# Kernel optimization log

Hardware: AMD Instinct MI355X
Metric: run time of the kernel (lower is better)

Reference implementation:

```python
import jax, jax.numpy as jnp
import numpy as np

NUM_TABLES = 26
NUM_ROWS = 50000
WIDTH = 128
BATCH = 4096
NNZ = 20
NUM_NUM = 13
MLP_SIZES = [512, 256, 128]


def setup_inputs() -> dict:
    key = jax.random.key(0)
    ks = jax.random.split(key, 16)
    numerical = jax.random.normal(ks[0], (BATCH, NUM_NUM), dtype=jnp.float32)
    cat = jax.random.randint(ks[1], (NUM_TABLES, BATCH, NNZ), 0, NUM_ROWS)
    tables = jax.random.normal(ks[2], (NUM_TABLES, NUM_ROWS, WIDTH), dtype=jnp.float32) * 0.01
    d_in = NUM_TABLES * WIDTH + NUM_NUM  # concat of pooled embeddings + numericals
    dims = [d_in] + MLP_SIZES + [1]
    inp = {"numerical": numerical, "cat": cat, "tables": tables}
    for i in range(len(dims) - 1):
        scale = 1.0 / np.sqrt(dims[i])
        inp[f"W{i+1}"] = jax.random.normal(ks[3 + i], (dims[i], dims[i + 1]), dtype=jnp.float32) * scale
        inp[f"b{i+1}"] = jnp.zeros((dims[i + 1],), dtype=jnp.float32)
    return inp


def reference(numerical, cat, tables, W1, b1, W2, b2, W3, b3, W4, b4):
    # Multi-table gather + reduce_sum: tables [T,R,W], cat [T,B,NNZ] -> pooled [T,B,W]
    pooled = jax.vmap(lambda T, idx: jnp.take(T, idx, axis=0).sum(axis=1))(tables, cat)
    # concat pooled tables (in input order) then numericals: [B, T*W + NUM_NUM]
    flat = pooled.transpose(1, 0, 2).reshape(pooled.shape[1], -1)
    x = jnp.concatenate([flat, numerical], axis=1)
    x = jax.nn.relu(x @ W1 + b1)
    x = jax.nn.relu(x @ W2 + b2)
    x = jax.nn.relu(x @ W3 + b3)
    return x @ W4 + b4  # [B, 1]
```

## Files before the change

### kernel.cpp

```cpp
#include <hip/hip_runtime.h>
#include <hip/hip_bf16.h>

#define T_NUM_TABLES 26
#define T_NUM_ROWS 50000
#define T_WIDTH 128
#define T_BATCH 4096
#define T_NNZ 20
#define T_NUM_NUM 13
#define T_DE (T_NUM_TABLES * T_WIDTH)

typedef __attribute__((ext_vector_type(4))) float f32x4;
typedef __attribute__((ext_vector_type(8))) short bf16x8;

__global__ void prep_v5(const float* __restrict__ W1, const float* __restrict__ W2,
                        const float* __restrict__ W3, const float* __restrict__ b1,
                        const float* __restrict__ b4, const float* __restrict__ num,
                        __hip_bfloat16* __restrict__ w1t, __hip_bfloat16* __restrict__ w2t,
                        __hip_bfloat16* __restrict__ w3t, float* __restrict__ c0,
                        float* __restrict__ out) {
  int bid = blockIdx.x;
  if (bid >= 1824) {
    int b = bid - 1824;
    __shared__ float snum[T_NUM_NUM];
    if (threadIdx.x < T_NUM_NUM) snum[threadIdx.x] = num[b * T_NUM_NUM + threadIdx.x];
    if (threadIdx.x == 0) out[b] = b4[0];
    __syncthreads();
#pragma unroll
    for (int rep = 0; rep < 2; ++rep) {
      int n = threadIdx.x + rep * 256;
      float acc = b1[n];
#pragma unroll
      for (int j = 0; j < T_NUM_NUM; ++j)
        acc += snum[j] * W1[(size_t)(T_DE + j) * 512 + n];
      c0[(size_t)b * 512 + n] = acc;
    }
    return;
  }
  const float* in;
  __hip_bfloat16* outt;
  int Kc, N, xb, yb;
  if (bid < 1664)      { in = W1; outt = w1t; Kc = 3328; N = 512; xb = bid % 104; yb = bid / 104; }
  else if (bid < 1792) { int r = bid - 1664; in = W2; outt = w2t; Kc = 512; N = 256; xb = r % 16; yb = r / 16; }
  else                 { int r = bid - 1792; in = W3; outt = w3t; Kc = 256; N = 128; xb = r % 8;  yb = r / 8;  }
  int tx = threadIdx.x & 31, ty = threadIdx.x >> 5;
  __shared__ float tile[32][33];
  int kb = xb * 32, nb = yb * 32;
  for (int r = ty; r < 32; r += 8) tile[r][tx] = in[(size_t)(kb + r) * N + nb + tx];
  __syncthreads();
  for (int r = ty; r < 32; r += 8) outt[(size_t)(nb + r) * Kc + kb + tx] = __float2bfloat16(tile[tx][r]);
}

__global__ void pool_v5(const float* __restrict__ tables,
                        const int* __restrict__ cat,
                        __hip_bfloat16* __restrict__ xh) {
  __shared__ int sidx[8][T_NNZ];
  const int b0 = blockIdx.x * 8;
  const int t = blockIdx.y;
  const int tx = threadIdx.x & 31;
  const int ty = threadIdx.x >> 5;
  if (threadIdx.x < 8 * T_NNZ) {
    int y = threadIdx.x / T_NNZ, j = threadIdx.x % T_NNZ;
    sidx[y][j] = cat[((size_t)t * T_BATCH + b0 + y) * T_NNZ + j];
  }
  __syncthreads();
  const f32x4* tb = (const f32x4*)(tables + (size_t)t * T_NUM_ROWS * T_WIDTH);
  f32x4 acc = {0.f, 0.f, 0.f, 0.f};
#pragma unroll
  for (int j = 0; j < T_NNZ; ++j) {
    acc += tb[(size_t)sidx[ty][j] * 32 + tx];
  }
  ushort4 u;
  {
    __hip_bfloat16 h0 = __float2bfloat16(acc[0]), h1 = __float2bfloat16(acc[1]);
    __hip_bfloat16 h2 = __float2bfloat16(acc[2]), h3 = __float2bfloat16(acc[3]);
    u.x = *(unsigned short*)&h0; u.y = *(unsigned short*)&h1;
    u.z = *(unsigned short*)&h2; u.w = *(unsigned short*)&h3;
  }
  *(ushort4*)(&xh[(size_t)(b0 + ty) * T_DE + t * T_WIDTH + tx * 4]) = u;
}

template <int BM, int BN, int RELU, int MODE>
__global__ __launch_bounds__(256, 2) void gemm_v5(
    const __hip_bfloat16* __restrict__ A,
    const __hip_bfloat16* __restrict__ Bt,
    const float* __restrict__ bias1,
    const float* __restrict__ bias2d,
    const float* __restrict__ W4,
    __hip_bfloat16* __restrict__ Ch,
    float* __restrict__ outv,
    int M, int N, int Kp) {
  constexpr int MR = BM / 32, NR = BN / 32;
  __shared__ char smem[BM * 128 + BN * 128];
  char* As = smem;
  char* Bs = smem + BM * 128;

  const int tid = threadIdx.x;
  const int wave = tid >> 6;
  const int lane = tid & 63;
  const int m0 = blockIdx.x * BM;
  const int n0 = blockIdx.y * BN;
  const int wr = wave >> 1;
  const int wc = wave & 1;

  f32x4 acc[MR][NR] = {};
  const size_t strideA = (size_t)Kp * 2;

  for (int k0 = 0; k0 < Kp; k0 += 64) {
    __syncthreads();
#pragma unroll
    for (int it = 0; it < BM / 32; ++it) {
      int chunk = wave + it * 4;
      int p = chunk * 1024 + lane * 16;
      int row = p >> 7;
      int colb = p & 127;
      int colb_g = colb ^ ((row & 7) << 4);
      size_t goff = (size_t)(m0 + row) * strideA + (size_t)k0 * 2 + colb_g;
      __builtin_amdgcn_global_load_lds(
          (const __attribute__((address_space(1))) void*)((const char*)A + goff),
          (__attribute__((address_space(3))) void*)(As + chunk * 1024), 16, 0, 0);
    }
#pragma unroll
    for (int it = 0; it < BN / 32; ++it) {
      int chunk = wave + it * 4;
      int p = chunk * 1024 + lane * 16;
      int row = p >> 7;
      int colb = p & 127;
      int colb_g = colb ^ ((row & 7) << 4);
      size_t goff = (size_t)(n0 + row) * strideA + (size_t)k0 * 2 + colb_g;
      __builtin_amdgcn_global_load_lds(
          (const __attribute__((address_space(1))) void*)((const char*)Bt + goff),
          (__attribute__((address_space(3))) void*)(Bs + chunk * 1024), 16, 0, 0);
    }
    __syncthreads();

#pragma unroll
    for (int ks = 0; ks < 2; ++ks) {
      bf16x8 af[MR], bfr[NR];
      const int cb = (ks * 32 + ((lane >> 4) * 8)) * 2;
#pragma unroll
      for (int m = 0; m < MR; ++m) {
        int row = wr * (BM / 2) + m * 16 + (lane & 15);
        int addr = row * 128 + (cb ^ ((row & 7) << 4));
        af[m] = *(const bf16x8*)(As + addr);
      }
#pragma unroll
      for (int n = 0; n < NR; ++n) {
        int row = wc * (BN / 2) + n * 16 + (lane & 15);
        int addr = row * 128 + (cb ^ ((row & 7) << 4));
        bfr[n] = *(const bf16x8*)(Bs + addr);
      }
#pragma unroll
      for (int m = 0; m < MR; ++m)
#pragma unroll
        for (int n = 0; n < NR; ++n)
          acc[m][n] = __builtin_amdgcn_mfma_f32_16x16x32_bf16(af[m], bfr[n], acc[m][n], 0, 0, 0);
    }
  }

#pragma unroll
  for (int m = 0; m < MR; ++m) {
#pragma unroll
    for (int n = 0; n < NR; ++n) {
      int col = n0 + wc * (BN / 2) + n * 16 + (lane & 15);
      float bv = bias1 ? bias1[col] : 0.f;
      float w4c = (MODE == 2) ? W4[col] : 0.f;
      float dot[4];
#pragma unroll
      for (int i = 0; i < 4; ++i) {
        int row = m0 + wr * (BM / 2) + m * 16 + ((lane >> 4) * 4) + i;
        float v = acc[m][n][i] + bv;
        if (bias2d) v += bias2d[(size_t)row * N + col];
        if (RELU) v = fmaxf(v, 0.f);
        if (MODE == 0) {
          Ch[(size_t)row * N + col] = __float2bfloat16(v);
        } else {
          dot[i] = v * w4c;
        }
      }
      if (MODE == 2) {
#pragma unroll
        for (int i = 0; i < 4; ++i) {
#pragma unroll
          for (int mask = 1; mask < 16; mask <<= 1) dot[i] += __shfl_xor(dot[i], mask);
        }
        if ((lane & 15) == 0) {
          int rowb = m0 + wr * (BM / 2) + m * 16 + ((lane >> 4) * 4);
#pragma unroll
          for (int i = 0; i < 4; ++i) atomicAdd(&outv[rowb + i], dot[i]);
        }
      }
    }
  }
}

extern "C" void kernel_launch(void* const* d_in, const int* in_sizes, int n_in,
                              void* d_out, int out_size, void* d_ws, size_t ws_size,
                              hipStream_t stream) {
  const float* numerical = (const float*)d_in[0];
  const int* cat = (const int*)d_in[1];
  const float* tables = (const float*)d_in[2];
  const float* W1 = (const float*)d_in[3];
  const float* b1 = (const float*)d_in[4];
  const float* W2 = (const float*)d_in[5];
  const float* b2 = (const float*)d_in[6];
  const float* W3 = (const float*)d_in[7];
  const float* b3 = (const float*)d_in[8];
  const float* W4 = (const float*)d_in[9];
  const float* b4 = (const float*)d_in[10];
  float* out = (float*)d_out;

  char* ws = (char*)d_ws;
  size_t off = 0;
  auto walloc = [&](size_t bytes) -> void* {
    void* p = ws + off;
    off = (off + bytes + 255) & ~(size_t)255;
    return p;
  };
  __hip_bfloat16* xh  = (__hip_bfloat16*)walloc((size_t)T_BATCH * T_DE * 2);
  __hip_bfloat16* w1t = (__hip_bfloat16*)walloc((size_t)512 * T_DE * 2);
  float*          c0  = (float*)walloc((size_t)T_BATCH * 512 * 4);
  __hip_bfloat16* a1  = (__hip_bfloat16*)walloc((size_t)T_BATCH * 512 * 2);
  __hip_bfloat16* w2t = (__hip_bfloat16*)walloc((size_t)256 * 512 * 2);
  __hip_bfloat16* a2  = (__hip_bfloat16*)walloc((size_t)T_BATCH * 256 * 2);
  __hip_bfloat16* w3t = (__hip_bfloat16*)walloc((size_t)128 * 256 * 2);

  prep_v5<<<1824 + T_BATCH, 256, 0, stream>>>(W1, W2, W3, b1, b4, numerical,
                                              w1t, w2t, w3t, c0, out);
  pool_v5<<<dim3(T_BATCH / 8, T_NUM_TABLES), 256, 0, stream>>>(tables, cat, xh);

  gemm_v5<64, 64, 1, 0><<<dim3(T_BATCH / 64, 512 / 64), 256, 0, stream>>>(
      xh, w1t, nullptr, c0, nullptr, a1, nullptr, T_BATCH, 512, T_DE);
  gemm_v5<64, 32, 1, 0><<<dim3(T_BATCH / 64, 256 / 32), 256, 0, stream>>>(
      a1, w2t, b2, nullptr, nullptr, a2, nullptr, T_BATCH, 256, 512);
  gemm_v5<64, 32, 1, 2><<<dim3(T_BATCH / 64, 128 / 32), 256, 0, stream>>>(
      a2, w3t, b3, nullptr, W4, nullptr, out, T_BATCH, 128, 256);
}
```

Measured before the change: 222.3 us.

## Merge pooling and weight prep into one launch; double-buffer GEMM LDS staging

Folds the embedding pooling kernel and the weight transpose/bias-prep kernel into a single launch with a flat block index, which removes one launch and lets the independent work run concurrently. The GEMM kernel now uses two LDS buffers so the global-to-LDS load for the next K tile is issued before the MFMA work on the current tile, with one barrier per iteration instead of two. This doubles shared memory per block, which may reduce occupancy. Correctness of the single-barrier scheme depends on the async global_load_lds writes finishing before that barrier.

```diff
diff --git a/kernel.cpp b/kernel.cpp
--- a/kernel.cpp
+++ b/kernel.cpp
@@ -12,16 +12,69 @@
 typedef __attribute__((ext_vector_type(4))) float f32x4;
 typedef __attribute__((ext_vector_type(8))) short bf16x8;
 
-__global__ void prep_v5(const float* __restrict__ W1, const float* __restrict__ W2,
-                        const float* __restrict__ W3, const float* __restrict__ b1,
-                        const float* __restrict__ b4, const float* __restrict__ num,
-                        __hip_bfloat16* __restrict__ w1t, __hip_bfloat16* __restrict__ w2t,
-                        __hip_bfloat16* __restrict__ w3t, float* __restrict__ c0,
-                        float* __restrict__ out) {
-  int bid = blockIdx.x;
-  if (bid >= 1824) {
-    int b = bid - 1824;
-    __shared__ float snum[T_NUM_NUM];
+#define PJ_POOL (512 * T_NUM_TABLES)
+#define PJ_WT (PJ_POOL + 1664 + 128 + 32)
+#define PJ_TOTAL (PJ_WT + T_BATCH)
+
+__global__ void poolprep_v6(const float* __restrict__ tables,
+                            const int* __restrict__ cat,
+                            const float* __restrict__ W1, const float* __restrict__ W2,
+                            const float* __restrict__ W3, const float* __restrict__ b1,
+                            const float* __restrict__ b4, const float* __restrict__ num,
+                            __hip_bfloat16* __restrict__ xh,
+                            __hip_bfloat16* __restrict__ w1t, __hip_bfloat16* __restrict__ w2t,
+                            __hip_bfloat16* __restrict__ w3t, float* __restrict__ c0,
+                            float* __restrict__ out) {
+  __shared__ int sidx[8][T_NNZ];
+  __shared__ float tile[32][33];
+  __shared__ float snum[T_NUM_NUM];
+  const int bid = blockIdx.x;
+
+  if (bid < PJ_POOL) {
+    const int g = bid & 511;
+    const int t = bid >> 9;
+    const int b0 = g * 8;
+    const int tx = threadIdx.x & 31;
+    const int ty = threadIdx.x >> 5;
+    if (threadIdx.x < 8 * T_NNZ) {
+      int y = threadIdx.x / T_NNZ, j = threadIdx.x % T_NNZ;
+      sidx[y][j] = cat[((size_t)t * T_BATCH + b0 + y) * T_NNZ + j];
+    }
+    __syncthreads();
+    const f32x4* tb = (const f32x4*)(tables + (size_t)t * T_NUM_ROWS * T_WIDTH);
+    f32x4 acc = {0.f, 0.f, 0.f, 0.f};
+#pragma unroll
+    for (int j = 0; j < T_NNZ; ++j) acc += tb[(size_t)sidx[ty][j] * 32 + tx];
+    ushort4 u;
+    {
+      __hip_bfloat16 h0 = __float2bfloat16(acc[0]), h1 = __float2bfloat16(acc[1]);
+      __hip_bfloat16 h2 = __float2bfloat16(acc[2]), h3 = __float2bfloat16(acc[3]);
+      u.x = *(unsigned short*)&h0; u.y = *(unsigned short*)&h1;
+      u.z = *(unsigned short*)&h2; u.w = *(unsigned short*)&h3;
+    }
+    *(ushort4*)(&xh[(size_t)(b0 + ty) * T_DE + t * T_WIDTH + tx * 4]) = u;
+    return;
+  }
+
+  if (bid < PJ_WT) {
+    int r = bid - PJ_POOL;
+    const float* in;
+    __hip_bfloat16* outt;
+    int Kc, N, xb, yb;
+    if (r < 1664)      { in = W1; outt = w1t; Kc = 3328; N = 512; xb = r % 104; yb = r / 104; }
+    else if (r < 1792) { r -= 1664; in = W2; outt = w2t; Kc = 512; N = 256; xb = r % 16; yb = r / 16; }
+    else               { r -= 1792; in = W3; outt = w3t; Kc = 256; N = 128; xb = r % 8;  yb = r / 8;  }
+    int tx = threadIdx.x & 31, ty = threadIdx.x >> 5;
+    int kb = xb * 32, nb = yb * 32;
+    for (int rr = ty; rr < 32; rr += 8) tile[rr][tx] = in[(size_t)(kb + rr) * N + nb + tx];
+    __syncthreads();
+    for (int rr = ty; rr < 32; rr += 8)
+      outt[(size_t)(nb + rr) * Kc + kb + tx] = __float2bfloat16(tile[tx][rr]);
+    return;
+  }
+
+  {
+    int b = bid - PJ_WT;
     if (threadIdx.x < T_NUM_NUM) snum[threadIdx.x] = num[b * T_NUM_NUM + threadIdx.x];
     if (threadIdx.x == 0) out[b] = b4[0];
     __syncthreads();
@@ -34,53 +87,11 @@
         acc += snum[j] * W1[(size_t)(T_DE + j) * 512 + n];
       c0[(size_t)b * 512 + n] = acc;
     }
-    return;
-  }
-  const float* in;
-  __hip_bfloat16* outt;
-  int Kc, N, xb, yb;
-  if (bid < 1664)      { in = W1; outt = w1t; Kc = 3328; N = 512; xb = bid % 104; yb = bid / 104; }
-  else if (bid < 1792) { int r = bid - 1664; in = W2; outt = w2t; Kc = 512; N = 256; xb = r % 16; yb = r / 16; }
-  else                 { int r = bid - 1792; in = W3; outt = w3t; Kc = 256; N = 128; xb = r % 8;  yb = r / 8;  }
-  int tx = threadIdx.x & 31, ty = threadIdx.x >> 5;
-  __shared__ float tile[32][33];
-  int kb = xb * 32, nb = yb * 32;
-  for (int r = ty; r < 32; r += 8) tile[r][tx] = in[(size_t)(kb + r) * N + nb + tx];
-  __syncthreads();
-  for (int r = ty; r < 32; r += 8) outt[(size_t)(nb + r) * Kc + kb + tx] = __float2bfloat16(tile[tx][r]);
+  }
 }
 
-__global__ void pool_v5(const float* __restrict__ tables,
-                        const int* __restrict__ cat,
-                        __hip_bfloat16* __restrict__ xh) {
-  __shared__ int sidx[8][T_NNZ];
-  const int b0 = blockIdx.x * 8;
-  const int t = blockIdx.y;
-  const int tx = threadIdx.x & 31;
-  const int ty = threadIdx.x >> 5;
-  if (threadIdx.x < 8 * T_NNZ) {
-    int y = threadIdx.x / T_NNZ, j = threadIdx.x % T_NNZ;
-    sidx[y][j] = cat[((size_t)t * T_BATCH + b0 + y) * T_NNZ + j];
-  }
-  __syncthreads();
-  const f32x4* tb = (const f32x4*)(tables + (size_t)t * T_NUM_ROWS * T_WIDTH);
-  f32x4 acc = {0.f, 0.f, 0.f, 0.f};
-#pragma unroll
-  for (int j = 0; j < T_NNZ; ++j) {
-    acc += tb[(size_t)sidx[ty][j] * 32 + tx];
-  }
-  ushort4 u;
-  {
-    __hip_bfloat16 h0 = __float2bfloat16(acc[0]), h1 = __float2bfloat16(acc[1]);
-    __hip_bfloat16 h2 = __float2bfloat16(acc[2]), h3 = __float2bfloat16(acc[3]);
-    u.x = *(unsigned short*)&h0; u.y = *(unsigned short*)&h1;
-    u.z = *(unsigned short*)&h2; u.w = *(unsigned short*)&h3;
-  }
-  *(ushort4*)(&xh[(size_t)(b0 + ty) * T_DE + t * T_WIDTH + tx * 4]) = u;
-}
-
 template <int BM, int BN, int RELU, int MODE>
-__global__ __launch_bounds__(256, 2) void gemm_v5(
+__global__ __launch_bounds__(256, 2) void gemm_v6(
     const __hip_bfloat16* __restrict__ A,
     const __hip_bfloat16* __restrict__ Bt,
     const float* __restrict__ bias1,
@@ -90,9 +101,8 @@
     float* __restrict__ outv,
     int M, int N, int Kp) {
   constexpr int MR = BM / 32, NR = BN / 32;
-  __shared__ char smem[BM * 128 + BN * 128];
-  char* As = smem;
-  char* Bs = smem + BM * 128;
+  constexpr int BUFB = BM * 128 + BN * 128;
+  __shared__ char smem[2 * BUFB];
 
   const int tid = threadIdx.x;
   const int wave = tid >> 6;
@@ -105,14 +115,14 @@
   f32x4 acc[MR][NR] = {};
   const size_t strideA = (size_t)Kp * 2;
 
-  for (int k0 = 0; k0 < Kp; k0 += 64) {
-    __syncthreads();
+  auto stage = [&](int k0, int buf) {
+    char* As = smem + buf * BUFB;
+    char* Bs = As + BM * 128;
 #pragma unroll
     for (int it = 0; it < BM / 32; ++it) {
       int chunk = wave + it * 4;
       int p = chunk * 1024 + lane * 16;
-      int row = p >> 7;
-      int colb = p & 127;
+      int row = p >> 7, colb = p & 127;
       int colb_g = colb ^ ((row & 7) << 4);
       size_t goff = (size_t)(m0 + row) * strideA + (size_t)k0 * 2 + colb_g;
       __builtin_amdgcn_global_load_lds(
@@ -123,16 +133,23 @@
     for (int it = 0; it < BN / 32; ++it) {
       int chunk = wave + it * 4;
       int p = chunk * 1024 + lane * 16;
-      int row = p >> 7;
-      int colb = p & 127;
+      int row = p >> 7, colb = p & 127;
       int colb_g = colb ^ ((row & 7) << 4);
       size_t goff = (size_t)(n0 + row) * strideA + (size_t)k0 * 2 + colb_g;
       __builtin_amdgcn_global_load_lds(
           (const __attribute__((address_space(1))) void*)((const char*)Bt + goff),
           (__attribute__((address_space(3))) void*)(Bs + chunk * 1024), 16, 0, 0);
     }
-    __syncthreads();
-
+  };
+
+  const int nt = Kp >> 6;
+  stage(0, 0);
+  __syncthreads();
+  int cur = 0;
+  for (int t = 0; t < nt; ++t) {
+    if (t + 1 < nt) stage((t + 1) << 6, cur ^ 1);
+    char* As = smem + cur * BUFB;
+    char* Bs = As + BM * 128;
 #pragma unroll
     for (int ks = 0; ks < 2; ++ks) {
       bf16x8 af[MR], bfr[NR];
@@ -155,6 +172,8 @@
         for (int n = 0; n < NR; ++n)
           acc[m][n] = __builtin_amdgcn_mfma_f32_16x16x32_bf16(af[m], bfr[n], acc[m][n], 0, 0, 0);
     }
+    __syncthreads();
+    cur ^= 1;
   }
 
 #pragma unroll
@@ -224,14 +243,13 @@
   __hip_bfloat16* a2  = (__hip_bfloat16*)walloc((size_t)T_BATCH * 256 * 2);
   __hip_bfloat16* w3t = (__hip_bfloat16*)walloc((size_t)128 * 256 * 2);
 
-  prep_v5<<<1824 + T_BATCH, 256, 0, stream>>>(W1, W2, W3, b1, b4, numerical,
-                                              w1t, w2t, w3t, c0, out);
-  pool_v5<<<dim3(T_BATCH / 8, T_NUM_TABLES), 256, 0, stream>>>(tables, cat, xh);
-
-  gemm_v5<64, 64, 1, 0><<<dim3(T_BATCH / 64, 512 / 64), 256, 0, stream>>>(
+  poolprep_v6<<<PJ_TOTAL, 256, 0, stream>>>(tables, cat, W1, W2, W3, b1, b4, numerical,
+                                            xh, w1t, w2t, w3t, c0, out);
+
+  gemm_v6<64, 64, 1, 0><<<dim3(T_BATCH / 64, 512 / 64), 256, 0, stream>>>(
       xh, w1t, nullptr, c0, nullptr, a1, nullptr, T_BATCH, 512, T_DE);
-  gemm_v5<64, 32, 1, 0><<<dim3(T_BATCH / 64, 256 / 32), 256, 0, stream>>>(
+  gemm_v6<64, 32, 1, 0><<<dim3(T_BATCH / 64, 256 / 32), 256, 0, stream>>>(
       a1, w2t, b2, nullptr, nullptr, a2, nullptr, T_BATCH, 256, 512);
-  gemm_v5<64, 32, 1, 2><<<dim3(T_BATCH / 64, 128 / 32), 256, 0, stream>>>(
+  gemm_v6<64, 32, 1, 2><<<dim3(T_BATCH / 64, 128 / 32), 256, 0, stream>>>(
       a2, w3t, b3, nullptr, W4, nullptr, out, T_BATCH, 128, 256);
 }
```

New measurement: 205.8 us. -7.4%, faster.
